# Kernel tuning notes

Measured on AMD Instinct MI355X. Metric: run time of the kernel, lower is better.

## Reference

```python
import jax, jax.numpy as jnp
import numpy as np
from jax import lax

EPS = 1e-5
DN = ('NCHW', 'OIHW', 'NCHW')

def _sign(v):
    # (v >= 0) * 2 - 1
    return jnp.where(v >= 0, 1.0, -1.0).astype(v.dtype)

def _conv(x, w, b):
    y = lax.conv_general_dilated(x, w, (1, 1), 'VALID', dimension_numbers=DN)
    return y + b[None, :, None, None]

def _bn(x):
    # BatchNorm2d(affine=False), training mode: biased batch stats over (N,H,W)
    m = jnp.mean(x, axis=(0, 2, 3), keepdims=True)
    v = jnp.var(x, axis=(0, 2, 3), keepdims=True)
    return (x - m) * lax.rsqrt(v + EPS)

def setup_inputs() -> dict:
    key = jax.random.key(0)
    ks = jax.random.split(key, 9)
    f = jnp.float32
    B = 8192
    x = jax.random.normal(ks[0], (B, 1, 28, 28), dtype=f)
    # conv params, clipped to [-1, 1] as in clip_weights()
    w1 = jnp.clip(jax.random.normal(ks[1], (32, 1, 9, 9), dtype=f) * 0.1, -1, 1)
    b1 = jnp.clip(jax.random.normal(ks[2], (32,), dtype=f) * 0.1, -1, 1)
    w2 = jnp.clip(jax.random.normal(ks[3], (16, 32, 9, 9), dtype=f) * 0.1, -1, 1)
    b2 = jnp.clip(jax.random.normal(ks[4], (16,), dtype=f) * 0.1, -1, 1)
    w3 = jnp.clip(jax.random.normal(ks[5], (8, 16, 9, 9), dtype=f) * 0.1, -1, 1)
    b3 = jnp.clip(jax.random.normal(ks[6], (8,), dtype=f) * 0.1, -1, 1)
    wl = jnp.clip(jax.random.normal(ks[7], (10, 8, 4, 4), dtype=f) * 0.1, -1, 1)
    bl = jnp.clip(jax.random.normal(ks[8], (10,), dtype=f) * 0.1, -1, 1)
    return {"x": x, "w1": w1, "b1": b1, "w2": w2, "b2": b2,
            "w3": w3, "b3": b3, "wl": wl, "bl": bl}

def _block(x, w, b, act=True, norm=True, binarized=True):
    if binarized:
        w, b = _sign(w), _sign(b)
    x = _conv(x, w, b)
    if norm:
        x = _bn(x)
    if act:
        x = _sign(x) if binarized else jax.nn.relu(x)
    return x

def reference(x, w1, b1, w2, b2, w3, b3, wl, bl):
    x = _sign(x)                        # binarize input activations
    x = _block(x, w1, b1)               # (B, 32, 20, 20)
    x = _block(x, w2, b2)               # (B, 16, 12, 12)
    x = _block(x, w3, b3)               # (B,  8,  4,  4)
    x = _block(x, wl, bl, act=False, norm=False)  # (B, 10, 1, 1), binarized weights
    return x.reshape(-1, 10)
```

## Files before the change

kernel.cpp:

```cpp
#include <hip/hip_runtime.h>
#include <stdint.h>

#define BATCH 8192
#define NVB   1024

#define OFF_W1R3  0
#define OFF_W2P   384
#define OFF_W3P   6144
#define OFF_WLB   9600
#define OFF_SBL   9760
#define OFF_TTOT  9856
#define OFF_S2P   341632
#define OFF_S3P   407168
#define OFF_Z2    440320
#define OFF_Z3    38189056

__global__ __launch_bounds__(256) void k1_pack_tsum(const float* __restrict__ x,
                                                    const float* __restrict__ w1,
                                                    const float* __restrict__ w2,
                                                    const float* __restrict__ w3,
                                                    const float* __restrict__ wl,
                                                    const float* __restrict__ bl,
                                                    uint8_t* __restrict__ ws) {
  const int tid = threadIdx.x;
  const int bid = blockIdx.x;
  int* Ttot = (int*)(ws + OFF_TTOT);

  if (bid < 4) {
    uint32_t* W2P = (uint32_t*)(ws + OFF_W2P);
    int e = bid * 162 + tid;
    if (tid < 162) {
      int och = e / 81, k = e % 81, kh = k / 9, kw = k % 9;
      uint32_t m0 = 0, m1 = 0;
      int oc0 = och * 2;
      #pragma unroll
      for (int ic = 0; ic < 32; ++ic) {
        if (w2[(oc0*32 + ic)*81 + k] < 0.f)     m0 |= 1u << ic;
        if (w2[((oc0+1)*32 + ic)*81 + k] < 0.f) m1 |= 1u << ic;
      }
      int idx = ((och*9 + kh)*10 + kw)*2;
      W2P[idx] = m0; W2P[idx+1] = m1;
    }
    if (bid == 0 && tid < 72) {
      int idx = (tid*10 + 9)*2;
      W2P[idx] = 0; W2P[idx+1] = 0;
    }
  } else if (bid < 7) {
    uint32_t* W3P = (uint32_t*)(ws + OFF_W3P);
    int e = (bid - 4) * 216 + tid;
    if (tid < 216) {
      int oc = e / 81, k = e % 81, kh = k / 9, kw = k % 9;
      uint32_t m = 0;
      #pragma unroll
      for (int ic = 0; ic < 16; ++ic)
        if (w3[(oc*16 + ic)*81 + k] < 0.f) m |= 1u << ic;
      W3P[(oc*9 + kh)*12 + kw] = m;
    }
    if (bid == 4 && tid < 216) { int row = tid / 3, p = tid % 3; W3P[row*12 + 9 + p] = 0; }
  } else if (bid == 7) {
    uint32_t* W1R3 = (uint32_t*)(ws + OFF_W1R3);
    if (tid < 96) {
      int oc = tid / 3, i = tid % 3;
      uint32_t m = 0;
      #pragma unroll
      for (int rr = 0; rr < 3; ++rr)
        #pragma unroll
        for (int kw = 0; kw < 9; ++kw)
          if (w1[oc*81 + (3*i+rr)*9 + kw] < 0.f) m |= 1u << (rr*9 + kw);
      W1R3[tid] = m;
    }
  } else if (bid == 8) {
    uint64_t* WLB = (uint64_t*)(ws + OFF_WLB);
    float* SBL = (float*)(ws + OFF_SBL);
    #pragma unroll
    for (int i = 0; i < 5; ++i) {
      int idx = i*256 + tid;
      float v = wl[idx];
      unsigned long long m = __ballot(v < 0.f);
      if ((tid & 63) == 0) WLB[idx >> 6] = m;
    }
    if (tid < 10) SBL[tid] = (bl[tid] >= 0.f) ? 1.f : -1.f;
  }

  __shared__ uint32_t rowm[224];
  __shared__ int Tacc[81];
  if (tid < 81) Tacc[tid] = 0;
  __syncthreads();
  const int img0 = bid * 8;
  if (tid < 224) {
    int il = tid / 28, r = tid % 28;
    const float4* xr = (const float4*)(x + (size_t)(img0 + il) * 784 + r * 28);
    uint32_t m = 0;
    #pragma unroll
    for (int j = 0; j < 7; ++j) {
      float4 v = xr[j];
      if (v.x < 0.f) m |= 1u << (j*4+0);
      if (v.y < 0.f) m |= 1u << (j*4+1);
      if (v.z < 0.f) m |= 1u << (j*4+2);
      if (v.w < 0.f) m |= 1u << (j*4+3);
    }
    rowm[tid] = m;
  }
  __syncthreads();
  if (tid < 72) {
    int il = tid / 9, kw = tid % 9;
    int base = il * 28;
    int n9[9];
    int sum20 = 0;
    #pragma unroll
    for (int r = 0; r < 20; ++r) {
      int n = __popc((rowm[base + r] >> kw) & 0xFFFFFu);
      if (r < 9) n9[r] = n;
      sum20 += n;
    }
    atomicAdd(&Tacc[kw], 400 - 2*sum20);
    #pragma unroll
    for (int kh = 1; kh <= 8; ++kh) {
      int nadd = __popc((rowm[base + kh + 19] >> kw) & 0xFFFFFu);
      sum20 += nadd - n9[kh-1];
      atomicAdd(&Tacc[kh*9 + kw], 400 - 2*sum20);
    }
  }
  __syncthreads();
  if (tid < 81) atomicAdd(&Ttot[tid], Tacc[tid]);
}

#define K2_IMGS 8
__global__ __launch_bounds__(256) void k2_conv12(const float* __restrict__ x,
                                                 uint8_t* __restrict__ ws) {
  const uint32_t* W1R3g = (const uint32_t*)(ws + OFF_W1R3);
  const uint32_t* W2Pg  = (const uint32_t*)(ws + OFF_W2P);
  const int* Ttot = (const int*)(ws + OFF_TTOT);
  int* S2P = (int*)(ws + OFF_S2P);

  __shared__ uint32_t __attribute__((aligned(16))) rowm[K2_IMGS*28];
  __shared__ uint32_t __attribute__((aligned(16))) w1r3[96];
  __shared__ uint32_t __attribute__((aligned(16))) w2p[1440];
  __shared__ int tlds[81];
  __shared__ int t1s[32];
  __shared__ uint32_t __attribute__((aligned(16))) A1s[K2_IMGS*400];
  __shared__ int s2acc[16];

  const int tid = threadIdx.x;
  const int img0 = blockIdx.x * K2_IMGS;

  for (int e = tid; e < 96; e += 256)   w1r3[e] = W1R3g[e];
  for (int e = tid; e < 1440; e += 256) w2p[e]  = W2Pg[e];
  if (tid < 81) tlds[tid] = Ttot[tid];
  if (tid < 16) s2acc[tid] = 0;
  if (tid < K2_IMGS*28) {
    int il = tid / 28, rr = tid % 28;
    const float4* xr = (const float4*)(x + (size_t)(img0 + il) * 784 + rr * 28);
    uint32_t m = 0;
    #pragma unroll
    for (int j = 0; j < 7; ++j) {
      float4 v = xr[j];
      if (v.x < 0.f) m |= 1u << (j*4+0);
      if (v.y < 0.f) m |= 1u << (j*4+1);
      if (v.z < 0.f) m |= 1u << (j*4+2);
      if (v.w < 0.f) m |= 1u << (j*4+3);
    }
    rowm[tid] = m;
  }
  __syncthreads();

  if (tid < 32) {
    long long S = 0;
    for (int kh = 0; kh < 9; ++kh)
      for (int kw = 0; kw < 9; ++kw) {
        int bit = (w1r3[tid*3 + kh/3] >> ((kh%3)*9 + kw)) & 1;
        S += (long long)(1 - 2*bit) * tlds[kh*9 + kw];
      }
    const long long N1 = (long long)BATCH * 400;
    long long q = S / N1, rr = S % N1;
    long long t = q + (rr > 0 ? 1 : 0);
    if ((t & 1) == 0) t += 1;
    t1s[tid] = (int)t;
  }
  __syncthreads();

  for (int G = tid; G < K2_IMGS*80; G += 256) {
    int il = G / 80, rem = G - il*80;
    int oh = rem >> 2, ow0 = (rem & 3) * 5;
    uint32_t R[9];
    #pragma unroll
    for (int i = 0; i < 9; ++i) R[i] = rowm[il*28 + oh + i];
    uint32_t win[5][3];
    #pragma unroll
    for (int j = 0; j < 5; ++j) {
      int ow = ow0 + j;
      #pragma unroll
      for (int i = 0; i < 3; ++i) {
        uint32_t b0 = (R[3*i]   >> ow) & 0x1FFu;
        uint32_t b1 = (R[3*i+1] >> ow) & 0x1FFu;
        uint32_t b2 = (R[3*i+2] >> ow) & 0x1FFu;
        win[j][i] = b0 | (b1 << 9) | (b2 << 18);
      }
    }
    uint32_t mask[5] = {0,0,0,0,0};
    #pragma unroll
    for (int ocg = 0; ocg < 4; ++ocg) {
      const uint4* wp = (const uint4*)&w1r3[ocg*24];
      uint32_t wr[24];
      #pragma unroll
      for (int q = 0; q < 6; ++q) {
        uint4 v = wp[q];
        wr[q*4+0]=v.x; wr[q*4+1]=v.y; wr[q*4+2]=v.z; wr[q*4+3]=v.w;
      }
      #pragma unroll
      for (int o8 = 0; o8 < 8; ++o8) {
        int oc = ocg*8 + o8;
        int t = t1s[oc];
        #pragma unroll
        for (int j = 0; j < 5; ++j) {
          int mm = __popc(win[j][0] ^ wr[o8*3])
                 + __popc(win[j][1] ^ wr[o8*3+1])
                 + __popc(win[j][2] ^ wr[o8*3+2]);
          mask[j] |= (uint32_t)((81 - 2*mm) < t) << oc;
        }
      }
    }
    #pragma unroll
    for (int j = 0; j < 5; ++j) A1s[il*400 + oh*20 + ow0 + j] = mask[j];
  }
  __syncthreads();

  uint32_t* Z2w = (uint32_t*)(ws + OFF_Z2);
  const int och = tid & 7, oc0 = och << 1;
  int sl0 = 0, sl1 = 0;
  for (int r = 0; r < 3; ++r) {
    int G = tid + r*256;
    int il = G / 96, rem = G - il*96;
    int oy = rem >> 3;
    const uint32_t* A = &A1s[il*400 + oy*20];
    int acc0[12], acc1[12];
    #pragma unroll
    for (int p = 0; p < 12; ++p) { acc0[p] = 0; acc1[p] = 0; }
    for (int kh = 0; kh < 9; ++kh) {
      const uint4* ar = (const uint4*)(A + kh*20);
      uint32_t a[20];
      #pragma unroll
      for (int q = 0; q < 5; ++q) {
        uint4 v = ar[q];
        a[q*4+0]=v.x; a[q*4+1]=v.y; a[q*4+2]=v.z; a[q*4+3]=v.w;
      }
      const uint4* wp4 = (const uint4*)&w2p[(och*9 + kh)*20];
      uint32_t wbuf[20];
      #pragma unroll
      for (int q = 0; q < 5; ++q) {
        uint4 v = wp4[q];
        wbuf[q*4+0]=v.x; wbuf[q*4+1]=v.y; wbuf[q*4+2]=v.z; wbuf[q*4+3]=v.w;
      }
      #pragma unroll
      for (int kw = 0; kw < 9; ++kw) {
        uint32_t w0 = wbuf[2*kw], w1v = wbuf[2*kw+1];
        #pragma unroll
        for (int px = 0; px < 12; ++px) {
          acc0[px] += __popc(a[kw+px] ^ w0);
          acc1[px] += __popc(a[kw+px] ^ w1v);
        }
      }
    }
    size_t wbase = (size_t)(img0+il)*1152 + (size_t)oy*96 + och;
    #pragma unroll
    for (int px = 0; px < 12; ++px) {
      int z0 = 2592 - 2*acc0[px], z1v = 2592 - 2*acc1[px];
      sl0 += z0; sl1 += z1v;
      Z2w[wbase + px*8] = (uint32_t)(uint16_t)(int16_t)z0
                        | ((uint32_t)(uint16_t)(int16_t)z1v << 16);
    }
  }
  atomicAdd(&s2acc[oc0],   sl0);
  atomicAdd(&s2acc[oc0+1], sl1);
  __syncthreads();
  if (tid < 16) S2P[blockIdx.x*16 + tid] = s2acc[tid];
}

#define K3_IMGS 8
__global__ __launch_bounds__(256) void k3_conv3(uint8_t* __restrict__ ws) {
  const int* S2P = (const int*)(ws + OFF_S2P);
  const uint32_t* W3Pg = (const uint32_t*)(ws + OFF_W3P);
  const uint32_t* Z2w = (const uint32_t*)(ws + OFF_Z2);
  uint32_t* Z3w = (uint32_t*)(ws + OFF_Z3);
  int* S3P = (int*)(ws + OFF_S3P);

  __shared__ uint32_t __attribute__((aligned(16))) w3p[864];
  __shared__ int part[256];
  __shared__ int t2s[16];
  __shared__ uint32_t __attribute__((aligned(16))) A2[K3_IMGS*144];
  __shared__ int s3acc[8];

  const int tid = threadIdx.x;
  const int img0 = blockIdx.x * K3_IMGS;

  {
    int c = tid & 15, g = tid >> 4;
    int s = 0;
    for (int j = 0; j < 64; ++j) s += S2P[(g + 16*j)*16 + c];
    part[tid] = s;
  }
  for (int e = tid; e < 864; e += 256) w3p[e] = W3Pg[e];
  if (tid < 8) s3acc[tid] = 0;
  __syncthreads();
  if (tid < 16) {
    long long S = 0;
    #pragma unroll
    for (int g = 0; g < 16; ++g) S += (long long)part[g*16 + tid];
    const long long N2 = (long long)BATCH * 144;
    long long q = S / N2, r = S % N2;
    long long t = q + (r > 0 ? 1 : 0);
    if (t & 1) t += 1;
    t2s[tid] = (int)t;
  }
  __syncthreads();

  for (int idx = tid; idx < K3_IMGS*144; idx += 256) {
    const uint4* zp = (const uint4*)&Z2w[(size_t)(img0 + idx/144)*1152 + (size_t)(idx%144)*8];
    uint4 v0 = zp[0], v1 = zp[1];
    uint32_t zz[8] = {v0.x,v0.y,v0.z,v0.w, v1.x,v1.y,v1.z,v1.w};
    uint32_t m = 0;
    #pragma unroll
    for (int i = 0; i < 8; ++i) {
      int zlo = (int)(short)(zz[i] & 0xFFFFu);
      int zhi = (int)zz[i] >> 16;
      m |= (uint32_t)(zlo < t2s[2*i])   << (2*i);
      m |= (uint32_t)(zhi < t2s[2*i+1]) << (2*i+1);
    }
    A2[idx] = m;
  }
  __syncthreads();

  const int il = tid >> 5, oc = (tid >> 2) & 7, oy = tid & 3;
  int acc[4] = {0, 0, 0, 0};
  #pragma unroll
  for (int kh = 0; kh < 9; ++kh) {
    const uint4* ar = (const uint4*)&A2[il*144 + (oy + kh)*12];
    uint4 v0 = ar[0], v1 = ar[1], v2 = ar[2];
    uint32_t a[12] = {v0.x,v0.y,v0.z,v0.w, v1.x,v1.y,v1.z,v1.w, v2.x,v2.y,v2.z,v2.w};
    const uint4* wr = (const uint4*)&w3p[(oc*9 + kh)*12];
    uint4 w0 = wr[0], w1v = wr[1], w2v = wr[2];
    uint32_t w[9] = {w0.x,w0.y,w0.z,w0.w, w1v.x,w1v.y,w1v.z,w1v.w, w2v.x};
    #pragma unroll
    for (int ox = 0; ox < 4; ++ox) {
      #pragma unroll
      for (int kw = 0; kw < 9; ++kw) acc[ox] += __popc(a[ox+kw] ^ w[kw]);
    }
  }
  int ssum = 0;
  uint32_t packed[2];
  #pragma unroll
  for (int h = 0; h < 2; ++h) {
    int za = 1296 - 2*acc[2*h], zb = 1296 - 2*acc[2*h+1];
    ssum += za + zb;
    packed[h] = (uint32_t)(uint16_t)(int16_t)za | ((uint32_t)(uint16_t)(int16_t)zb << 16);
  }
  *(uint2*)&Z3w[(size_t)(img0 + il)*64 + oc*8 + oy*2] = make_uint2(packed[0], packed[1]);
  atomicAdd(&s3acc[oc], ssum);
  __syncthreads();
  if (tid < 8) S3P[blockIdx.x*8 + tid] = s3acc[tid];
}

__global__ __launch_bounds__(64) void k4_final(uint8_t* __restrict__ ws,
                                               float* __restrict__ out) {
  const uint32_t* Z3w = (const uint32_t*)(ws + OFF_Z3);
  const int* S3P = (const int*)(ws + OFF_S3P);
  const uint64_t* WLBg = (const uint64_t*)(ws + OFF_WLB);
  const float* SBLg = (const float*)(ws + OFF_SBL);
  __shared__ int red[64];
  __shared__ int t3[8];
  __shared__ uint64_t wlb[20];
  __shared__ float sbl[10];
  const int tid = threadIdx.x;
  {
    int oc = tid & 7, g = tid >> 3;
    int s = 0;
    for (int b = g; b < NVB; b += 8) s += S3P[b*8 + oc];
    red[tid] = s;
  }
  if (tid < 20) wlb[tid] = WLBg[tid];
  if (tid >= 32 && tid < 42) sbl[tid - 32] = SBLg[tid - 32];
  __syncthreads();
  if (tid < 8) {
    long long S = 0;
    #pragma unroll
    for (int g = 0; g < 8; ++g) S += (long long)red[g*8 + tid];
    const long long N3 = (long long)BATCH * 16;
    long long q = S / N3, r = S % N3;
    long long t = q + (r > 0 ? 1 : 0);
    if (t & 1) t += 1;
    t3[tid] = (int)t;
  }
  __syncthreads();
  int img = blockIdx.x * 64 + tid;
  const uint4* zp = (const uint4*)&Z3w[(size_t)img * 64];
  uint32_t zz[64];
  #pragma unroll
  for (int q = 0; q < 16; ++q) {
    uint4 v = zp[q];
    zz[q*4+0]=v.x; zz[q*4+1]=v.y; zz[q*4+2]=v.z; zz[q*4+3]=v.w;
  }
  uint64_t a0 = 0, a1 = 0;
  #pragma unroll
  for (int j = 0; j < 64; ++j) {
    int z = (j & 1) ? ((int)zz[j>>1] >> 16) : (int)(short)(zz[j>>1] & 0xFFFFu);
    a0 |= (uint64_t)(z < t3[j >> 4]) << j;
  }
  #pragma unroll
  for (int j = 0; j < 64; ++j) {
    int z = (j & 1) ? ((int)zz[32 + (j>>1)] >> 16) : (int)(short)(zz[32 + (j>>1)] & 0xFFFFu);
    a1 |= (uint64_t)(z < t3[(64 + j) >> 4]) << j;
  }
  #pragma unroll
  for (int oc = 0; oc < 10; ++oc) {
    int mism = __popcll(a0 ^ wlb[oc*2]) + __popcll(a1 ^ wlb[oc*2 + 1]);
    out[(size_t)img*10 + oc] = (float)(128 - 2*mism) + sbl[oc];
  }
}

extern "C" void kernel_launch(void* const* d_in, const int* in_sizes, int n_in,
                              void* d_out, int out_size, void* d_ws, size_t ws_size,
                              hipStream_t stream) {
  (void)in_sizes; (void)n_in; (void)out_size; (void)ws_size;
  const float* x  = (const float*)d_in[0];
  const float* w1 = (const float*)d_in[1];
  const float* w2 = (const float*)d_in[3];
  const float* w3 = (const float*)d_in[5];
  const float* wl = (const float*)d_in[7];
  const float* bl = (const float*)d_in[8];
  uint8_t* ws = (uint8_t*)d_ws;
  float* out = (float*)d_out;

  hipMemsetAsync(ws + OFF_TTOT, 0, 324, stream);
  k1_pack_tsum<<<1024, 256, 0, stream>>>(x, w1, w2, w3, wl, bl, ws);
  k2_conv12<<<1024, 256, 0, stream>>>(x, ws);
  k3_conv3<<<1024, 256, 0, stream>>>(ws);
  k4_final<<<128, 64, 0, stream>>>(ws, out);
}
```

Baseline: 271.8 us.

## Process 32 images per conv3 block with per-thread full output tiles

The conv3 kernel now handles 32 images per block instead of 8, and each thread computes all 16 output pixels for one image and channel. Every A2 row is loaded once and reused across the output rows that need it. This cuts the number of blocks and the repeated partial-sum reductions over S2P, and the wider stores write 32 bytes per thread. The final kernel is rescaled to 256-thread blocks over the smaller partial-sum array. In exchange each thread holds more registers and the grid shrinks to 256 blocks, which lowers parallelism.

```diff
diff --git a/kernel.cpp b/kernel.cpp
--- a/kernel.cpp
+++ b/kernel.cpp
@@ -276,7 +276,6 @@
   if (tid < 16) S2P[blockIdx.x*16 + tid] = s2acc[tid];
 }
 
-#define K3_IMGS 8
 __global__ __launch_bounds__(256) void k3_conv3(uint8_t* __restrict__ ws) {
   const int* S2P = (const int*)(ws + OFF_S2P);
   const uint32_t* W3Pg = (const uint32_t*)(ws + OFF_W3P);
@@ -287,11 +286,11 @@
   __shared__ uint32_t __attribute__((aligned(16))) w3p[864];
   __shared__ int part[256];
   __shared__ int t2s[16];
-  __shared__ uint32_t __attribute__((aligned(16))) A2[K3_IMGS*144];
+  __shared__ uint32_t __attribute__((aligned(16))) A2[32*144];
   __shared__ int s3acc[8];
 
   const int tid = threadIdx.x;
-  const int img0 = blockIdx.x * K3_IMGS;
+  const int img0 = blockIdx.x * 32;
 
   {
     int c = tid & 15, g = tid >> 4;
@@ -314,7 +313,9 @@
   }
   __syncthreads();
 
-  for (int idx = tid; idx < K3_IMGS*144; idx += 256) {
+  #pragma unroll
+  for (int j = 0; j < 18; ++j) {
+    int idx = tid + j*256;
     const uint4* zp = (const uint4*)&Z2w[(size_t)(img0 + idx/144)*1152 + (size_t)(idx%144)*8];
     uint4 v0 = zp[0], v1 = zp[1];
     uint32_t zz[8] = {v0.x,v0.y,v0.z,v0.w, v1.x,v1.y,v1.z,v1.w};
@@ -330,38 +331,50 @@
   }
   __syncthreads();
 
-  const int il = tid >> 5, oc = (tid >> 2) & 7, oy = tid & 3;
-  int acc[4] = {0, 0, 0, 0};
-  #pragma unroll
-  for (int kh = 0; kh < 9; ++kh) {
-    const uint4* ar = (const uint4*)&A2[il*144 + (oy + kh)*12];
+  const int il = tid >> 3, oc = tid & 7;
+  int acc[16];
+  #pragma unroll
+  for (int i = 0; i < 16; ++i) acc[i] = 0;
+  #pragma unroll
+  for (int r = 0; r < 12; ++r) {
+    const uint4* ar = (const uint4*)&A2[il*144 + r*12];
     uint4 v0 = ar[0], v1 = ar[1], v2 = ar[2];
     uint32_t a[12] = {v0.x,v0.y,v0.z,v0.w, v1.x,v1.y,v1.z,v1.w, v2.x,v2.y,v2.z,v2.w};
-    const uint4* wr = (const uint4*)&w3p[(oc*9 + kh)*12];
-    uint4 w0 = wr[0], w1v = wr[1], w2v = wr[2];
-    uint32_t w[9] = {w0.x,w0.y,w0.z,w0.w, w1v.x,w1v.y,w1v.z,w1v.w, w2v.x};
-    #pragma unroll
-    for (int ox = 0; ox < 4; ++ox) {
-      #pragma unroll
-      for (int kw = 0; kw < 9; ++kw) acc[ox] += __popc(a[ox+kw] ^ w[kw]);
+    #pragma unroll
+    for (int oy = 0; oy < 4; ++oy) {
+      if (r - oy >= 0 && r - oy <= 8) {
+        int kh = r - oy;
+        const uint4* wr = (const uint4*)&w3p[(oc*9 + kh)*12];
+        uint4 w0 = wr[0], w1v = wr[1], w2v = wr[2];
+        uint32_t w[9] = {w0.x,w0.y,w0.z,w0.w, w1v.x,w1v.y,w1v.z,w1v.w, w2v.x};
+        #pragma unroll
+        for (int ox = 0; ox < 4; ++ox) {
+          int m = 0;
+          #pragma unroll
+          for (int kw = 0; kw < 9; ++kw) m += __popc(a[ox+kw] ^ w[kw]);
+          acc[oy*4+ox] += m;
+        }
+      }
     }
   }
   int ssum = 0;
-  uint32_t packed[2];
-  #pragma unroll
-  for (int h = 0; h < 2; ++h) {
+  uint32_t packed[8];
+  #pragma unroll
+  for (int h = 0; h < 8; ++h) {
     int za = 1296 - 2*acc[2*h], zb = 1296 - 2*acc[2*h+1];
     ssum += za + zb;
     packed[h] = (uint32_t)(uint16_t)(int16_t)za | ((uint32_t)(uint16_t)(int16_t)zb << 16);
   }
-  *(uint2*)&Z3w[(size_t)(img0 + il)*64 + oc*8 + oy*2] = make_uint2(packed[0], packed[1]);
+  uint4* zp = (uint4*)&Z3w[(size_t)(img0 + il)*64 + oc*8];
+  zp[0] = make_uint4(packed[0], packed[1], packed[2], packed[3]);
+  zp[1] = make_uint4(packed[4], packed[5], packed[6], packed[7]);
   atomicAdd(&s3acc[oc], ssum);
   __syncthreads();
   if (tid < 8) S3P[blockIdx.x*8 + tid] = s3acc[tid];
 }
 
-__global__ __launch_bounds__(64) void k4_final(uint8_t* __restrict__ ws,
-                                               float* __restrict__ out) {
+__global__ __launch_bounds__(256) void k4_final(uint8_t* __restrict__ ws,
+                                                float* __restrict__ out) {
   const uint32_t* Z3w = (const uint32_t*)(ws + OFF_Z3);
   const int* S3P = (const int*)(ws + OFF_S3P);
   const uint64_t* WLBg = (const uint64_t*)(ws + OFF_WLB);
@@ -371,14 +384,14 @@
   __shared__ uint64_t wlb[20];
   __shared__ float sbl[10];
   const int tid = threadIdx.x;
-  {
+  if (tid < 64) {
     int oc = tid & 7, g = tid >> 3;
     int s = 0;
-    for (int b = g; b < NVB; b += 8) s += S3P[b*8 + oc];
+    for (int b = g; b < 256; b += 8) s += S3P[b*8 + oc];
     red[tid] = s;
   }
-  if (tid < 20) wlb[tid] = WLBg[tid];
-  if (tid >= 32 && tid < 42) sbl[tid - 32] = SBLg[tid - 32];
+  if (tid >= 64 && tid < 84) wlb[tid - 64] = WLBg[tid - 64];
+  if (tid >= 96 && tid < 106) sbl[tid - 96] = SBLg[tid - 96];
   __syncthreads();
   if (tid < 8) {
     long long S = 0;
@@ -391,7 +404,7 @@
     t3[tid] = (int)t;
   }
   __syncthreads();
-  int img = blockIdx.x * 64 + tid;
+  int img = blockIdx.x * 256 + tid;
   const uint4* zp = (const uint4*)&Z3w[(size_t)img * 64];
   uint32_t zz[64];
   #pragma unroll
@@ -433,6 +446,6 @@
   hipMemsetAsync(ws + OFF_TTOT, 0, 324, stream);
   k1_pack_tsum<<<1024, 256, 0, stream>>>(x, w1, w2, w3, wl, bl, ws);
   k2_conv12<<<1024, 256, 0, stream>>>(x, ws);
-  k3_conv3<<<1024, 256, 0, stream>>>(ws);
-  k4_final<<<128, 64, 0, stream>>>(ws, out);
+  k3_conv3<<<256, 256, 0, stream>>>(ws);
+  k4_final<<<32, 256, 0, stream>>>(ws, out);
 }
```

Measured after the change: 259.2 us. -4.6%, faster.
